# Performance work log

Hardware: AMD Instinct MI355X
Metric: run time of the kernel (lower is better)

## Reference

```python
import jax, jax.numpy as jnp
import numpy as np
from math import factorial

# ---- architecture constants (from S2ConvNet_original.__init__) ----
B_IN, B_L1, B_L2 = 30, 15, 10
F1, F2, NCLS = 20, 40, 10
BATCH = 32

# ---------- numpy precompute: Wigner small-d matrices and quadrature ----------

def wigner_d(l, beta):
    """Wigner small-d matrix d^l_{m,n}(beta) for all m,n, vectorized over beta.
    Returns [len(beta), 2l+1, 2l+1] with centered indices (row m+l, col n+l)."""
    beta = np.atleast_1d(np.asarray(beta, dtype=np.float64))
    cb, sb = np.cos(beta / 2), np.sin(beta / 2)
    d = np.zeros((beta.size, 2 * l + 1, 2 * l + 1))
    for m in range(-l, l + 1):
        for n in range(-l, l + 1):
            pref = np.sqrt(float(factorial(l + m) * factorial(l - m) * factorial(l + n) * factorial(l - n)))
            s = np.zeros_like(beta)
            for k in range(max(0, m - n), min(l + m, l - n) + 1):
                c = (-1.0) ** k / float(factorial(k) * factorial(l + m - k) * factorial(l - n - k) * factorial(n - m + k))
                s += c * cb ** (2 * l + m - n - 2 * k) * sb ** (n - m + 2 * k)
            d[:, m + l, n + l] = pref * s
    return d

def wigner_stack(nl, betas):
    """Zero-padded stack of d^l matrices: [nl, n_beta, 2nl-1, 2nl-1], centered at nl-1."""
    M, c = 2 * nl - 1, nl - 1
    D = np.zeros((nl, len(betas), M, M))
    for l in range(nl):
        D[l, :, c - l:c + l + 1, c - l:c + l + 1] = wigner_d(l, betas)
    return D

def dh_weights(b):
    """Driscoll-Healy / SOFT quadrature weights over the 2b beta samples."""
    j = np.arange(2 * b); k = np.arange(b)
    s = (np.sin(np.outer(2 * j + 1, 2 * k + 1) * np.pi / (4 * b)) / (2 * k + 1)).sum(axis=1)
    return (2.0 / b) * np.sin(np.pi * (2 * j + 1) / (4 * b)) * s

def soft_betas(b):
    return np.pi * (2 * np.arange(2 * b) + 1) / (4 * b)

def centered_freqs(nl, n):
    # map centered m in [-(nl-1), nl-1] to fft bin indices of length-n transform
    return (np.arange(2 * nl - 1) - (nl - 1)) % n

# ---- conv1 (S2 -> SO3), b_in=30, b_out=15 ----
NL1, M1 = B_L1, 2 * B_L1 - 1
_D1F = wigner_stack(NL1, soft_betas(B_IN))[:, :, :, NL1 - 1] * dh_weights(B_IN)[None, :, None]  # [15,60,29]
_D1I = wigner_stack(NL1, soft_betas(B_L1))  # [15,30,29,29]
FQI1 = centered_freqs(NL1, 2 * B_IN)
FQO1 = centered_freqs(NL1, 2 * B_L1)
# s2_near_identity_grid: max_beta=pi/8, n_alpha=8, n_beta=3 -> 24 points
_gb = np.arange(1, 4) * (np.pi / 8) / 3
_ga = np.linspace(0, 2 * np.pi, 8, endpoint=False)
GB1, GA1 = [g.ravel() for g in np.meshgrid(_gb, _ga, indexing='ij')]
_m1 = np.arange(M1) - (NL1 - 1)
_Y1 = ((2 * np.arange(NL1) + 1.0)[:, None, None]
       * wigner_stack(NL1, GB1)[:, :, :, NL1 - 1].transpose(0, 2, 1)
       * np.exp(-1j * np.outer(_m1, GA1))[None])  # [15,29,24] spherical-harmonic basis at grid

# ---- conv2 (SO3 -> SO3), b_in=15, b_out=10 ----
NL2, M2 = B_L2, 2 * B_L2 - 1
_D2F = wigner_stack(NL2, soft_betas(B_L1)) * dh_weights(B_L1)[None, :, None, None]  # [10,30,19,19]
_D2I = wigner_stack(NL2, soft_betas(B_L2))  # [10,20,19,19]
FQI2 = centered_freqs(NL2, 2 * B_L1)
FQO2 = centered_freqs(NL2, 2 * B_L2)
# so3_near_identity_grid: 3 betas x 8 alphas x 8 gammas = 192 points
_gg = np.linspace(0, 2 * np.pi, 8, endpoint=False)
GB2, GA2, GG2 = [g.ravel() for g in np.meshgrid(_gb, _ga, _gg, indexing='ij')]
_m2 = np.arange(M2) - (NL2 - 1)
_Y2 = ((2 * np.arange(NL2) + 1.0)[:, None, None, None]
       * wigner_stack(NL2, GB2).transpose(0, 2, 3, 1)
       * np.exp(-1j * (np.outer(_m2, GA2)[:, None, :] + np.outer(_m2, GG2)[None, :, :]))[None])  # [10,19,19,192]

D1F = jnp.asarray(_D1F, jnp.float32); D1I = jnp.asarray(_D1I, jnp.float32); Y1 = jnp.asarray(_Y1, jnp.complex64)
D2F = jnp.asarray(_D2F, jnp.float32); D2I = jnp.asarray(_D2I, jnp.float32); Y2 = jnp.asarray(_Y2, jnp.complex64)
W_INT = jnp.asarray(dh_weights(B_L2), jnp.float32)  # [20]


def s2_conv(x, w, bias):
    # x: [B,1,60,60] (beta, alpha) -> SO3 signal [B,F1,30,30,30]
    xf = jnp.fft.fft(x, axis=-1)[..., FQI1]                       # [B,1,60,29] alpha-FFT, centered m
    X = jnp.einsum('bfjm,ljm->bflm', xf, D1F)                      # S2 FT: [B,1,15,29]
    psi = jnp.einsum('iog,lmg->lmio', w, Y1)                       # kernel S2 FT: [15,29,1,20]
    Z = jnp.einsum('bilm,lnio->bolmn', X, jnp.conj(psi))           # outer product m x n: [B,20,15,29,29]
    Fb = jnp.einsum('bolmn,ljmn->bojmn', Z, D1I)                   # beta synthesis: [B,20,30,29,29]
    n = 2 * B_L1
    full = jnp.zeros(Fb.shape[:3] + (n, n), Fb.dtype).at[..., FQO1[:, None], FQO1[None, :]].set(Fb)
    y = jnp.fft.ifft2(full, axes=(-2, -1)).real * (n * n)          # inverse alpha/gamma FFT
    return y + bias


def so3_conv(x, w, bias):
    # x: [B,F1,30,30,30] (beta, alpha, gamma) -> [B,F2,20,20,20]
    xf = jnp.fft.fft2(x, axes=(-2, -1))[..., FQI2[:, None], FQI2[None, :]]  # [B,20,30,19,19]
    X = jnp.einsum('bfjmn,ljmn->bflmn', xf, D2F)                   # SO3 FT: [B,20,10,19,19]
    psi = jnp.einsum('iog,lmng->lmnio', w, Y2)                     # kernel SO3 FT: [10,19,19,20,40]
    Z = jnp.einsum('bilmn,lknio->bolmk', X, jnp.conj(psi))         # Z^l = X^l @ Psi^l^H: [B,40,10,19,19]
    Fb = jnp.einsum('bolmk,ljmk->bojmk', Z, D2I)                   # [B,40,20,19,19]
    n = 2 * B_L2
    full = jnp.zeros(Fb.shape[:3] + (n, n), Fb.dtype).at[..., FQO2[:, None], FQO2[None, :]].set(Fb)
    y = jnp.fft.ifft2(full, axes=(-2, -1)).real * (n * n)
    return y + bias


def setup_inputs() -> dict:
    key = jax.random.key(0)
    ks = jax.random.split(key, 6)
    x = jax.random.normal(ks[0], (BATCH, 1, 2 * B_IN, 2 * B_IN), jnp.float32)
    w1 = jax.random.normal(ks[1], (1, F1, GB1.size), jnp.float32) / np.sqrt(GB1.size)
    b1 = jax.random.normal(ks[2], (1, F1, 1, 1, 1), jnp.float32) * 0.01
    w2 = jax.random.normal(ks[3], (F1, F2, GB2.size), jnp.float32) / np.sqrt(F1 * GB2.size)
    b2 = jax.random.normal(ks[4], (1, F2, 1, 1, 1), jnp.float32) * 0.01
    w_lin = jax.random.normal(ks[5], (NCLS, F2), jnp.float32) / np.sqrt(F2)
    bl_lin = jnp.zeros((NCLS,), jnp.float32)
    return {"x": x, "w1": w1, "b1": b1, "w2": w2, "b2": b2, "w_lin": w_lin, "bl_lin": bl_lin}


def reference(x, w1, b1, w2, b2, w_lin, bl_lin):
    h = jax.nn.relu(s2_conv(x, w1, b1))                            # [B,20,30,30,30]
    h = jax.nn.relu(so3_conv(h, w2, b2))                           # [B,40,20,20,20]
    # so3_integrate: quadrature over beta, uniform sums over alpha/gamma
    g = jnp.einsum('bfjkl,j->bf', h, W_INT) * (2 * np.pi / (2 * B_L2)) ** 2
    return g @ w_lin.T + bl_lin                                    # [B,10]
```

## Files before the change

### kernel.cpp

```cpp
#include <hip/hip_runtime.h>
#include <cmath>
#include <cstdio>

#ifndef M_PI
#define M_PI 3.14159265358979323846
#endif

#define OFF_D1F 0
#define OFF_D1I 26100
#define OFF_Y1  404550
#define OFF_D2F 425430
#define OFF_D2I 533730
#define OFF_WI  605930
#define OFF_E1  605950
#define OFF_I1  609430
#define OFF_E2  611170
#define OFF_I2  612310
#define OFF_DHW30 613070
#define OFF_DHW15 613130
#define NCONST  613160

#define WOFF_CONST 0ul
#define WOFF_Y2BF  2457600ul
#define WOFF_W2BF  5406720ul
#define WOFF_AAUG  5750784ul
#define WOFF_BT    15581184ul
#define WOFF_H1    39174144ul
#define WOFF_CPSI  39174144ul
#define WOFF_Z     39174144ul
#define WOFF_H2    2457600ul
#define WOFF_XF1   76140544ul
#define WOFF_X1    (76140544ul + 445440ul)
#define WOFF_PSI1  (76140544ul + 445440ul + 111360ul)
#define WOFF_G     (76140544ul + 445440ul + 111360ul + 69600ul)
#define WS_NEED    (WOFF_G + 5120ul)

typedef __attribute__((ext_vector_type(8))) short short8v;
typedef __attribute__((ext_vector_type(4))) float f32x4;

__device__ inline unsigned short f2bf(float x){
  unsigned int u = __float_as_uint(x);
  u += 0x7FFFu + ((u >> 16) & 1u);
  return (unsigned short)(u >> 16);
}
__device__ inline float bf2f(unsigned short u){
  return __uint_as_float(((unsigned int)u) << 16);
}

__device__ inline double dfact(int n){ double r=1.0; for(int i=2;i<=n;i++) r*=(double)i; return r; }
__device__ inline double dpowi(double x,int e){ double r=1.0; for(int i=0;i<e;i++) r*=x; return r; }
__device__ double wig(int l,int m,int n,double beta){
  if(m < -l || m > l || n < -l || n > l) return 0.0;
  double cb=cos(0.5*beta), sb=sin(0.5*beta);
  double pref=sqrt(dfact(l+m)*dfact(l-m)*dfact(l+n)*dfact(l-n));
  int k0 = (m-n)>0 ? (m-n) : 0;
  int k1 = (l+m) < (l-n) ? (l+m) : (l-n);
  double c0 = ((k0&1)?-1.0:1.0)/(dfact(k0)*dfact(l+m-k0)*dfact(l-n-k0)*dfact(n-m+k0));
  double t = c0 * dpowi(cb, 2*l+m-n-2*k0) * dpowi(sb, n-m+2*k0);
  double ratio = (sb*sb)/(cb*cb);
  double s = t;
  for(int k=k0;k<k1;k++){
    t *= -((double)(l+m-k)*(double)(l-n-k)) / ((double)(k+1)*(double)(n-m+k+1)) * ratio;
    s += t;
  }
  return pref*s;
}
__device__ inline double dh_w(int b,int j){
  double s=0.0;
  for(int k=0;k<b;k++) s += sin((2.0*j+1.0)*(2.0*k+1.0)*M_PI/(4.0*b))/(2.0*k+1.0);
  return (2.0/b)*sin(M_PI*(2.0*j+1.0)/(4.0*b))*s;
}
__device__ inline double soft_beta(int b,int j){ return M_PI*(2.0*j+1.0)/(4.0*b); }
__device__ inline void octcs(int q, double* c, double* s){
  const double r = 0.70710678118654752440;
  int i = q & 7;
  const double C[8]={1.0,r,0.0,-r,-1.0,-r,0.0,r};
  const double S[8]={0.0,r,1.0,r,0.0,-r,-1.0,-r};
  *c=C[i]; *s=S[i];
}

__global__ __launch_bounds__(256) void kconst0(float* __restrict__ C){
  for(int idx = blockIdx.x*256 + threadIdx.x; idx < 3670; idx += gridDim.x*256){
    if(idx < 20){ C[OFF_WI+idx]=(float)dh_w(10,idx); }
    else if(idx < 80){ int j=idx-20; C[OFF_DHW30+j]=(float)dh_w(30,j); }
    else if(idx < 110){ int j=idx-80; C[OFF_DHW15+j]=(float)dh_w(15,j); }
    else if(idx < 1850){ int q=idx-110;
      int a=q%60; int m=q/60; double ph=-2.0*M_PI*(double)(m-14)*a/60.0;
      C[OFF_E1+2*q]=(float)cos(ph); C[OFF_E1+2*q+1]=(float)sin(ph);
    } else if(idx < 2720){ int q=idx-1850;
      int m=q%29; int p=q/29; double ph=2.0*M_PI*(double)p*(double)(m-14)/30.0;
      C[OFF_I1+2*q]=(float)cos(ph); C[OFF_I1+2*q+1]=(float)sin(ph);
    } else if(idx < 3290){ int q=idx-2720;
      int a=q%30; int m=q/30; double ph=-2.0*M_PI*(double)(m-9)*a/30.0;
      C[OFF_E2+2*q]=(float)cos(ph); C[OFF_E2+2*q+1]=(float)sin(ph);
    } else { int q=idx-3290;
      int m=q%19; int p=q/19; double ph=2.0*M_PI*(double)p*(double)(m-9)/20.0;
      C[OFF_I2+2*q]=(float)cos(ph); C[OFF_I2+2*q+1]=(float)sin(ph);
    }
  }
}

__global__ __launch_bounds__(256) void kconst(float* __restrict__ C,
                                              unsigned int* __restrict__ Y2p){
  for(long idx = (long)blockIdx.x*blockDim.x + threadIdx.x; idx < 1332770L;
      idx += (long)gridDim.x*blockDim.x){
    if(idx < 26100L){
      int m=(int)(idx%29); int j=(int)((idx/29)%60); int l=(int)(idx/(29*60));
      C[OFF_D1F+idx] = (float)( wig(l, m-14, 0, soft_beta(30,j)) * (double)C[OFF_DHW30+j] );
    } else if(idx < 404550L){ long q=idx-26100L;
      int n=(int)(q%29); int m=(int)((q/29)%29); int j=(int)((q/841)%30); int l=(int)(q/(841*30));
      C[OFF_D1I+q] = (float)wig(l, m-14, n-14, soft_beta(15,j));
    } else if(idx < 414990L){ long q=idx-404550L;
      int g=(int)(q%24); int m=(int)((q/24)%29); int l=(int)(q/(24*29));
      double gb=((g>>3)+1)*(M_PI/8.0)/3.0;
      int ka = g&7;
      double mag=(2*l+1)*wig(l, m-14, 0, gb);
      double cc,ss; octcs((m-14)*ka, &cc, &ss);
      C[OFF_Y1+2*q]  =(float)(mag*cc);
      C[OFF_Y1+2*q+1]=(float)(-mag*ss);
    } else if(idx < 523290L){ long q=idx-414990L;
      int n=(int)(q%19); int m=(int)((q/19)%19); int j=(int)((q/361)%30); int l=(int)(q/(361*30));
      C[OFF_D2F+q]=(float)( wig(l,m-9,n-9,soft_beta(15,j)) * (double)C[OFF_DHW15+j] );
    } else if(idx < 595490L){ long q=idx-523290L;
      int n=(int)(q%19); int m=(int)((q/19)%19); int j=(int)((q/361)%20); int l=(int)(q/(361*20));
      C[OFF_D2I+q]=(float)wig(l,m-9,n-9,soft_beta(10,j));
    } else { long q=idx-595490L;
      int g2=(int)(q%96); int row=(int)((q/96)%768); int l=(int)(q/(96*768));
      unsigned int outv=0u;
      if(row<722){
        int kn=row>>1, ri=row&1, kk=kn/19, n=kn%19;
        int g0=2*g2;
        double gb=((g0>>6)+1)*(M_PI/8.0)/3.0;
        double mag=(2*l+1)*wig(l,kk-9,n-9,gb);
        int ka=(g0>>3)&7;
        double c0,s0,c1,s1;
        octcs((kk-9)*ka + (n-9)*(g0&7), &c0,&s0);
        octcs((kk-9)*ka + (n-9)*((g0+1)&7), &c1,&s1);
        float v0 = ri ? (float)(-mag*s0) : (float)(mag*c0);
        float v1 = ri ? (float)(-mag*s1) : (float)(mag*c1);
        outv = (unsigned int)f2bf(v0) | (((unsigned int)f2bf(v1))<<16);
      }
      Y2p[q]=outv;
    }
  }
}

__global__ __launch_bounds__(256) void kfill(uint4* __restrict__ p, long n16){
  uint4 z; z.x=0u; z.y=0u; z.z=0u; z.w=0u;
  for(long i=(long)blockIdx.x*256+threadIdx.x; i<n16; i+=(long)gridDim.x*256) p[i]=z;
}

__global__ __launch_bounds__(256) void kw2(const float* __restrict__ w2,
                                           unsigned int* __restrict__ w2bf){
  int idx = blockIdx.x*256 + threadIdx.x;
  if(idx >= 896*96) return;
  int row=idx/96, g2=idx%96;
  float a=0.f, b=0.f;
  if(row<800){ a=w2[row*192+2*g2]; b=w2[row*192+2*g2+1]; }
  w2bf[idx] = (unsigned int)f2bf(a) | (((unsigned int)f2bf(b))<<16);
}


__global__ __launch_bounds__(256) void k1a(const float* __restrict__ x,
                                           const float2* __restrict__ E1,
                                           float2* __restrict__ xf1){
  int idx = blockIdx.x*256 + threadIdx.x;
  if(idx >= 32*60*29) return;
  int m = idx % 29; int bj = idx / 29;
  const float* row = x + bj*60;
  float sr=0.f, si=0.f;
  for(int a=0;a<60;a++){ float2 e=E1[m*60+a]; float v=row[a]; sr+=v*e.x; si+=v*e.y; }
  xf1[idx] = make_float2(sr,si);
}

__global__ __launch_bounds__(256) void k1b(const float2* __restrict__ xf1,
                                           const float* __restrict__ D1F,
                                           float2* __restrict__ X1){
  int idx = blockIdx.x*256 + threadIdx.x;
  if(idx >= 32*15*29) return;
  int m = idx % 29; int lb = idx / 29; int l = lb % 15; int b = lb / 15;
  float sr=0.f, si=0.f;
  for(int j=0;j<60;j++){
    float d = D1F[(l*60+j)*29+m]; float2 v = xf1[(b*60+j)*29+m];
    sr += d*v.x; si += d*v.y;
  }
  X1[(b*15+l)*29+m] = make_float2(sr,si);
}

__global__ __launch_bounds__(256) void kpsi1(const float* __restrict__ w1,
                                             const float2* __restrict__ Y1,
                                             float2* __restrict__ psi1cO){
  int idx = blockIdx.x*256 + threadIdx.x;
  if(idx >= 15*29*20) return;
  int o = idx % 20; int ln = idx / 20;
  float sr=0.f, si=0.f;
  for(int g=0;g<24;g++){ float w=w1[o*24+g]; float2 y=Y1[ln*24+g]; sr+=w*y.x; si+=w*y.y; }
  psi1cO[o*435 + ln] = make_float2(sr,-si);
}

__global__ __launch_bounds__(512) void k2(const float2* __restrict__ X1,
                                          const float2* __restrict__ psi1cO,
                                          const float* __restrict__ D1I,
                                          const float2* __restrict__ I1g,
                                          const float* __restrict__ b1,
                                          unsigned short* __restrict__ h1){
  int o=blockIdx.x, b=blockIdx.y;
  __shared__ float2 sX[15][29];
  __shared__ float2 sP[15][29];
  __shared__ __align__(16) unsigned short I1A[64][72];
  __shared__ __align__(16) unsigned short I1C[32][72];
  __shared__ __align__(16) unsigned short An[32][72];
  __shared__ __align__(16) unsigned short Tl[32][72];
  int t=threadIdx.x;
  for(int q=t;q<435;q+=512){ ((float2*)sX)[q]=X1[b*435+q]; ((float2*)sP)[q]=psi1cO[o*435+q]; }
  for(int q=t;q<64*72;q+=512){
    int R=q/72, k=q%72; float v=0.f;
    if(k<64){ int kk=k&31, kh=k>>5;
      if(kk<29){
        if(R<30){ float2 e=I1g[R*29+kk]; v = kh ? -e.y : e.x; }
        else if(R>=32 && R<62){ float2 e=I1g[(R-32)*29+kk]; v = kh ? e.x : e.y; }
      }
    }
    I1A[R][k]=f2bf(v);
  }
  for(int q=t;q<32*72;q+=512){
    int Qr=q/72, k=q%72; float v=0.f;
    if(Qr<30 && k<64){ int kk=k&31, kh=k>>5;
      if(kk<29){ float2 e=I1g[Qr*29+kk]; v = kh ? -e.y : e.x; }
    }
    I1C[Qr][k]=f2bf(v);
  }
  for(int q=t;q<32*72;q+=512){ An[q/72][q%72]=0; Tl[q/72][q%72]=0; }
  __syncthreads();
  float Pr[2][15], Pi[2][15];
  #pragma unroll
  for(int s=0;s<2;s++){
    int id=t+512*s;
    if(id<841){
      int m=id/29, n=id%29;
      #pragma unroll
      for(int l=0;l<15;l++){
        float2 xx=sX[l][m], pp=sP[l][n];
        Pr[s][l]=xx.x*pp.x-xx.y*pp.y;
        Pi[s][l]=xx.x*pp.y+xx.y*pp.x;
      }
    }
  }
  int wid=t>>6, lane=t&63;
  int fr=lane&15, ko=(lane>>4)*8;
  int mwB=wid>>1, nwB=wid&1;
  short8v aB0 = *(const short8v*)&I1A[16*mwB+fr][ko];
  short8v aB1 = *(const short8v*)&I1A[16*mwB+fr][32+ko];
  int mwC=(wid>>1)&1, nwC=wid&1;
  short8v bC0 = *(const short8v*)&I1C[16*nwC+fr][ko];
  short8v bC1 = *(const short8v*)&I1C[16*nwC+fr][32+ko];
  float bias=b1[o];
  for(int j=0;j<30;j++){
    #pragma unroll
    for(int s=0;s<2;s++){
      int id=t+512*s;
      if(id<841){
        const float* dp = D1I + j*841 + id;
        float ar=0.f, ai=0.f;
        #pragma unroll
        for(int l=0;l<15;l++){ float d=dp[l*25230]; ar+=Pr[s][l]*d; ai+=Pi[s][l]*d; }
        int m=id/29, n=id%29;
        An[n][m]   =f2bf(ar);
        An[n][32+m]=f2bf(ai);
      }
    }
    __syncthreads();
    f32x4 accB={0.f,0.f,0.f,0.f};
    short8v b0 = *(const short8v*)&An[16*nwB+fr][ko];
    short8v b1v= *(const short8v*)&An[16*nwB+fr][32+ko];
    accB=__builtin_amdgcn_mfma_f32_16x16x32_bf16(aB0,b0,accB,0,0,0);
    accB=__builtin_amdgcn_mfma_f32_16x16x32_bf16(aB1,b1v,accB,0,0,0);
    #pragma unroll
    for(int r=0;r<4;r++){
      int R=16*mwB+(lane>>4)*4+r;
      int cc=16*nwB+fr;
      Tl[R&31][(R>>5)*32+cc]=f2bf(accB[r]);
    }
    __syncthreads();
    if(wid<4){
      f32x4 accC={0.f,0.f,0.f,0.f};
      short8v a0 = *(const short8v*)&Tl[16*mwC+fr][ko];
      short8v a1 = *(const short8v*)&Tl[16*mwC+fr][32+ko];
      accC=__builtin_amdgcn_mfma_f32_16x16x32_bf16(a0,bC0,accC,0,0,0);
      accC=__builtin_amdgcn_mfma_f32_16x16x32_bf16(a1,bC1,accC,0,0,0);
      size_t base=((size_t)(b*20+o)*30+j)*900;
      #pragma unroll
      for(int r=0;r<4;r++){
        int p=16*mwC+(lane>>4)*4+r, qq=16*nwC+fr;
        if(p<30 && qq<30){
          float v=fmaxf(accC[r]+bias,0.f);
          h1[base+p*30+qq]=f2bf(v);
        }
      }
    }
  }
}

__global__ __launch_bounds__(256) void k3g(const unsigned short* __restrict__ A,
                                           const unsigned short* __restrict__ B,
                                           float* __restrict__ Cf){
  int l = blockIdx.z;
  int m0 = blockIdx.y*128, n0 = blockIdx.x*128;
  __shared__ unsigned short As[128][40];
  __shared__ unsigned short Bs[128][40];
  int t = threadIdx.x;
  int wid = t>>6, lane = t&63;
  int wr = wid>>1, wc = wid&1;
  f32x4 acc[4][4];
  #pragma unroll
  for(int a=0;a<4;a++)
    #pragma unroll
    for(int c=0;c<4;c++) acc[a][c]=(f32x4){0.f,0.f,0.f,0.f};
  const unsigned short* Ag = A;
  const unsigned short* Bg = B + (size_t)l*768*192;
  int row_a = wr*64 + (lane&15);
  int row_b = wc*64 + (lane&15);
  int ko = (lane>>4)*8;
  for(int kt=0; kt<192; kt+=32){
    #pragma unroll
    for(int it=0; it<2; it++){
      int q = t + 256*it;
      int r = q>>2, c8 = (q&3)*8;
      *(uint4*)&As[r][c8] = *(const uint4*)&Ag[(size_t)(m0+r)*192 + kt + c8];
      *(uint4*)&Bs[r][c8] = *(const uint4*)&Bg[(size_t)(n0+r)*192 + kt + c8];
    }
    __syncthreads();
    short8v af[4], bfv[4];
    #pragma unroll
    for(int f=0; f<4; f++){
      af[f]  = *(const short8v*)&As[row_a + f*16][ko];
      bfv[f] = *(const short8v*)&Bs[row_b + f*16][ko];
    }
    #pragma unroll
    for(int fm=0;fm<4;fm++)
      #pragma unroll
      for(int fn=0;fn<4;fn++)
        acc[fm][fn] = __builtin_amdgcn_mfma_f32_16x16x32_bf16(af[fm], bfv[fn], acc[fm][fn], 0,0,0);
    __syncthreads();
  }
  #pragma unroll
  for(int fm=0;fm<4;fm++){
    int mb = m0 + wr*64 + fm*16 + ((lane>>4)*4);
    #pragma unroll
    for(int fn=0;fn<4;fn++){
      int n = n0 + wc*64 + fn*16 + (lane&15);
      #pragma unroll
      for(int r=0;r<4;r++){
        Cf[((size_t)(l*896)+mb+r)*768 + n] = acc[fm][fn][r];
      }
    }
  }
}

__global__ __launch_bounds__(384) void kBt(const float* __restrict__ Cf,
                                           unsigned short* __restrict__ Bt){
  int c = blockIdx.x;
  int l = blockIdx.y;
  int t = threadIdx.x;
  if(t>=380) return;
  int i=t/19, n=t%19;
  int o=c/19, kk=c%19;
  float2 v = *(const float2*)&Cf[((size_t)(l*896) + i*40+o)*768 + (kk*19+n)*2];
  float zr = v.x, zi = -v.y;
  unsigned short* base = Bt + (size_t)l*1536*768;
  size_t r0=(size_t)(2*c)*768, r1=r0+768;
  int col=i*19+n;
  base[r0+col]     = f2bf(zr);
  base[r0+384+col] = f2bf(-zi);
  base[r1+col]     = f2bf(zi);
  base[r1+384+col] = f2bf(zr);
}

__global__ __launch_bounds__(512) void k4(const unsigned short* __restrict__ h1,
                                          const float* __restrict__ D2F,
                                          const float2* __restrict__ E2g,
                                          unsigned short* __restrict__ Aaug){
  int i=blockIdx.x, b=blockIdx.y;
  __shared__ __align__(16) unsigned short E2c[48][32];
  __shared__ __align__(16) unsigned short E2A[48][64];
  __shared__ __align__(16) unsigned short T1[192][72];
  __shared__ __align__(16) unsigned short U2[192][44];
  int t=threadIdx.x;
  for(int q=t;q<48*32;q+=512){
    int R=q>>5, g=q&31; float v=0.f;
    if(R<38 && g<30){ float2 e=E2g[(R%19)*30+g]; v=(R<19)? e.x : e.y; }
    E2c[R][g]=f2bf(v);
  }
  for(int q=t;q<48*64;q+=512){
    int R=q>>6, c=q&63; float v=0.f;
    if(R<38){
      int mm=R%19; int mi=(R>=19);
      if(c<30){ float2 e=E2g[mm*30+c]; v = mi ? e.y : e.x; }
      else if(c>=32 && c<62){ float2 e=E2g[mm*30+(c-32)]; v = mi ? e.x : -e.y; }
    }
    E2A[R][c]=f2bf(v);
  }
  for(int q=t;q<192*72;q+=512) T1[q/72][q%72]=0;
  for(int q=t;q<192*44;q+=512) U2[q/44][q%44]=0;
  float accr[10], acci[10];
  #pragma unroll
  for(int l=0;l<10;l++){ accr[l]=0.f; acci[l]=0.f; }
  int m3=t/19, n3=t%19;
  int wid=t>>6, lane=t&63, fr=lane&15, fc=lane&15, ko=(lane>>4)*8, rq=(lane>>4)*4;
  size_t blk=(size_t)(b*20+i)*27000;
  const unsigned int* h1u=(const unsigned int*)h1;
  __syncthreads();
  for(int p=0;p<3;p++){
    int j0=p*10;
    for(int mt=wid; mt<19; mt+=8){
      int rg=16*mt+fr;
      size_t base=blk + (size_t)j0*900 + (size_t)rg*30 + ko;
      union{ unsigned int u[4]; short8v v; } A;
      const unsigned int* pp=h1u + (base>>1);
      A.u[0]=pp[0]; A.u[1]=pp[1]; A.u[2]=pp[2]; A.u[3]=pp[3];
      #pragma unroll
      for(int nt=0;nt<3;nt++){
        short8v Bf=*(const short8v*)&E2c[16*nt+fr][ko];
        f32x4 ac={0.f,0.f,0.f,0.f};
        ac=__builtin_amdgcn_mfma_f32_16x16x32_bf16(A.v,Bf,ac,0,0,0);
        int np=16*nt+fc;
        if(np<38){
          int ri=(np>=19), nn=np-19*ri;
          #pragma unroll
          for(int r=0;r<4;r++){
            int rgw=16*mt+rq+r;
            if(rgw<300){
              int jr=rgw/30, a=rgw%30;
              T1[jr*19+nn][32*ri+a]=f2bf(ac[r]);
            }
          }
        }
      }
    }
    __syncthreads();
    for(int u=0;u<5;u++){
      int tile=wid+8*u; if(tile>=36) break;
      int mt2=tile/12, nt2=tile%12;
      short8v a0=*(const short8v*)&E2A[16*mt2+fr][ko];
      short8v a1=*(const short8v*)&E2A[16*mt2+fr][32+ko];
      short8v b0=*(const short8v*)&T1[16*nt2+fr][ko];
      short8v b1=*(const short8v*)&T1[16*nt2+fr][32+ko];
      f32x4 ac={0.f,0.f,0.f,0.f};
      ac=__builtin_amdgcn_mfma_f32_16x16x32_bf16(a0,b0,ac,0,0,0);
      ac=__builtin_amdgcn_mfma_f32_16x16x32_bf16(a1,b1,ac,0,0,0);
      int jn=16*nt2+fc;
      if(jn<190){
        #pragma unroll
        for(int r=0;r<4;r++){
          int R=16*mt2+rq+r;
          if(R<38) U2[jn][R]=f2bf(ac[r]);
        }
      }
    }
    __syncthreads();
    if(t<361){
      for(int jr=0;jr<10;jr++){
        int jg=j0+jr;
        const float* dp=D2F + (size_t)jg*361 + t;
        float xr=bf2f(U2[jr*19+n3][m3]);
        float xi=bf2f(U2[jr*19+n3][19+m3]);
        #pragma unroll
        for(int l=0;l<10;l++){ float d=dp[l*10830]; accr[l]+=d*xr; acci[l]+=d*xi; }
      }
    }
  }
  if(t<361){
    #pragma unroll
    for(int l=0;l<10;l++){
      size_t row=((size_t)(l*640) + b*19+m3)*768;
      Aaug[row + i*19+n3]       = f2bf(accr[l]);
      Aaug[row + 384 + i*19+n3] = f2bf(acci[l]);
    }
  }
}

__global__ __launch_bounds__(256) void k5(const unsigned short* __restrict__ A,
                                          const unsigned short* __restrict__ B,
                                          float* __restrict__ Cf){
  int l = blockIdx.z;
  int m0 = blockIdx.y*128, n0 = blockIdx.x*128;
  __shared__ unsigned short As[128][40];
  __shared__ unsigned short Bs[128][40];
  int t = threadIdx.x;
  int wid = t>>6, lane = t&63;
  int wr = wid>>1, wc = wid&1;
  f32x4 acc[4][4];
  #pragma unroll
  for(int a=0;a<4;a++)
    #pragma unroll
    for(int c=0;c<4;c++) acc[a][c]=(f32x4){0.f,0.f,0.f,0.f};
  const unsigned short* Ag = A + (size_t)l*640*768;
  const unsigned short* Bg = B + (size_t)l*1536*768;
  int row_a = wr*64 + (lane&15);
  int row_b = wc*64 + (lane&15);
  int ko = (lane>>4)*8;
  for(int kt=0; kt<768; kt+=32){
    #pragma unroll
    for(int it=0; it<2; it++){
      int q = t + 256*it;
      int r = q>>2, c8 = (q&3)*8;
      *(uint4*)&As[r][c8] = *(const uint4*)&Ag[(size_t)(m0+r)*768 + kt + c8];
      *(uint4*)&Bs[r][c8] = *(const uint4*)&Bg[(size_t)(n0+r)*768 + kt + c8];
    }
    __syncthreads();
    short8v af[4], bfv[4];
    #pragma unroll
    for(int f=0; f<4; f++){
      af[f]  = *(const short8v*)&As[row_a + f*16][ko];
      bfv[f] = *(const short8v*)&Bs[row_b + f*16][ko];
    }
    #pragma unroll
    for(int fm=0;fm<4;fm++)
      #pragma unroll
      for(int fn=0;fn<4;fn++)
        acc[fm][fn] = __builtin_amdgcn_mfma_f32_16x16x32_bf16(af[fm], bfv[fn], acc[fm][fn], 0,0,0);
    __syncthreads();
  }
  #pragma unroll
  for(int fm=0;fm<4;fm++){
    int mb = m0 + wr*64 + fm*16 + ((lane>>4)*4);
    #pragma unroll
    for(int fn=0;fn<4;fn++){
      int n = n0 + wc*64 + fn*16 + (lane&15);
      if(n<1520){
        #pragma unroll
        for(int r=0;r<4;r++){
          int m = mb + r;
          if(m<608) Cf[((size_t)(l*608)+m)*1520 + n] = acc[fm][fn][r];
        }
      }
    }
  }
}

__global__ __launch_bounds__(512) void k6(const float2* __restrict__ Z,
                                          const float* __restrict__ D2I,
                                          const float2* __restrict__ I2g,
                                          const float* __restrict__ b2,
                                          unsigned short* __restrict__ h2){
  int o=blockIdx.x, b=blockIdx.y;
  __shared__ __align__(16) unsigned short U[29952];
  __shared__ __align__(16) unsigned short I2A[48][72];
  __shared__ __align__(16) unsigned short I2C[32][72];
  int t=threadIdx.x;
  for(int q=t;q<14976;q+=512) ((unsigned int*)U)[q]=0u;
  for(int q=t;q<48*72;q+=512){
    int R=q/72, kd=q%72; float v=0.f;
    if(kd<38){
      int mm = (kd<19)? kd : kd-19; int hi = (kd>=19);
      if(R<20){ float2 e=I2g[R*19+mm]; v = hi ? -e.y : e.x; }
      else if(R<40){ float2 e=I2g[(R-20)*19+mm]; v = hi ? e.x : e.y; }
    }
    I2A[R][kd]=f2bf(v);
  }
  for(int q=t;q<32*72;q+=512){
    int Qr=q/72, kd=q%72; float v=0.f;
    if(Qr<20 && kd<38){
      int kk2 = (kd<19)? kd : kd-19; int hi = (kd>=19);
      float2 e=I2g[Qr*19+kk2]; v = hi ? -e.y : e.x;
    }
    I2C[Qr][kd]=f2bf(v);
  }
  float zr[10], zi[10];
  int m=t/19, kk=t%19;
  if(t<361){
    #pragma unroll
    for(int l=0;l<10;l++){
      float2 z=Z[(size_t)(l*608 + b*19+m)*760 + o*19+kk];
      zr[l]=z.x; zi[l]=z.y;
    }
  }
  __syncthreads();
  if(t<361){
    for(int j=0;j<20;j++){
      float ar=0.f, ai=0.f;
      const float* dp = D2I + j*361 + t;
      #pragma unroll
      for(int l=0;l<10;l++){ float d=dp[l*7220]; ar+=zr[l]*d; ai+=zi[l]*d; }
      U[(j*19+kk)*72 + m]      = f2bf(ar);
      U[(j*19+kk)*72 + 19 + m] = f2bf(ai);
    }
  }
  __syncthreads();
  int wid=t>>6, lane=t&63, fr=lane&15, ko=(lane>>4)*8;
  f32x4 acc1[9];
  #pragma unroll
  for(int u=0;u<9;u++){
    int tile=wid+8*u;
    int mt=tile/24, nt=tile%24;
    short8v a0=*(const short8v*)&I2A[16*mt+fr][ko];
    short8v a1=*(const short8v*)&I2A[16*mt+fr][32+ko];
    short8v bb0=*(const short8v*)&U[(16*nt+fr)*72+ko];
    short8v bb1=*(const short8v*)&U[(16*nt+fr)*72+32+ko];
    f32x4 ac={0.f,0.f,0.f,0.f};
    ac=__builtin_amdgcn_mfma_f32_16x16x32_bf16(a0,bb0,ac,0,0,0);
    ac=__builtin_amdgcn_mfma_f32_16x16x32_bf16(a1,bb1,ac,0,0,0);
    acc1[u]=ac;
  }
  __syncthreads();
  #pragma unroll
  for(int u=0;u<9;u++){
    int tile=wid+8*u; int mt=tile/24, nt=tile%24;
    #pragma unroll
    for(int r=0;r<4;r++){
      int R=16*mt+(lane>>4)*4+r;
      int n=16*nt+fr;
      if(R<40 && n<380){
        int j=n/19, kq=n%19;
        U[(j*20 + (R%20))*72 + (R/20)*19 + kq] = f2bf(acc1[u][r]);
      }
    }
  }
  __syncthreads();
  float bias=b2[o];
  size_t obase=((size_t)b*40+o)*8000;
  #pragma unroll
  for(int u=0;u<7;u++){
    int tile=wid+8*u;
    if(tile<52){
      int mt=tile>>1, nt=tile&1;
      short8v a0=*(const short8v*)&U[(16*mt+fr)*72+ko];
      short8v a1=*(const short8v*)&U[(16*mt+fr)*72+32+ko];
      short8v bb0=*(const short8v*)&I2C[16*nt+fr][ko];
      short8v bb1=*(const short8v*)&I2C[16*nt+fr][32+ko];
      f32x4 ac={0.f,0.f,0.f,0.f};
      ac=__builtin_amdgcn_mfma_f32_16x16x32_bf16(a0,bb0,ac,0,0,0);
      ac=__builtin_amdgcn_mfma_f32_16x16x32_bf16(a1,bb1,ac,0,0,0);
      #pragma unroll
      for(int r=0;r<4;r++){
        int row=16*mt+(lane>>4)*4+r;
        int q=16*nt+fr;
        if(row<400 && q<20){
          float v=fmaxf(ac[r]+bias,0.f);
          h2[obase + row*20 + q]=f2bf(v);
        }
      }
    }
  }
}

__global__ __launch_bounds__(256) void k7a(const unsigned int* __restrict__ h2p,
                                           const float* __restrict__ WI,
                                           float* __restrict__ g){
  int bf=blockIdx.x;
  const unsigned int* base=h2p + (size_t)bf*4000;
  int t=threadIdx.x; float s=0.f;
  for(int q=t;q<4000;q+=256){
    unsigned int v=base[q];
    float w=WI[q/200];
    s += (bf2f((unsigned short)(v&0xFFFF))+bf2f((unsigned short)(v>>16)))*w;
  }
  __shared__ float red[256];
  red[t]=s; __syncthreads();
  for(int off=128;off>0;off>>=1){ if(t<off) red[t]+=red[t+off]; __syncthreads(); }
  if(t==0){
    const float c=(float)((2.0*M_PI/20.0)*(2.0*M_PI/20.0));
    g[bf]=red[0]*c;
  }
}

__global__ __launch_bounds__(64) void k7b(const float* __restrict__ g,
                                          const float* __restrict__ wlin,
                                          const float* __restrict__ bl,
                                          float* __restrict__ out){
  int idx=blockIdx.x*64+threadIdx.x;
  if(idx>=320) return;
  int b=idx/10, c=idx%10;
  float s=bl[c];
  for(int f=0;f<40;f++) s += g[b*40+f]*wlin[c*40+f];
  out[b*10+c]=s;
}

extern "C" void kernel_launch(void* const* d_in, const int* in_sizes, int n_in,
                              void* d_out, int out_size, void* d_ws, size_t ws_size,
                              hipStream_t stream){
  (void)in_sizes; (void)n_in; (void)out_size;
  const float* x    = (const float*)d_in[0];
  const float* w1   = (const float*)d_in[1];
  const float* b1   = (const float*)d_in[2];
  const float* w2   = (const float*)d_in[3];
  const float* b2   = (const float*)d_in[4];
  const float* wlin = (const float*)d_in[5];
  const float* bl   = (const float*)d_in[6];
  float* out = (float*)d_out;
  char*  ws  = (char*)d_ws;

  if(ws_size < WS_NEED){
    fprintf(stderr, "kernel_launch: ws too small: have %zu need %lu\n", ws_size, WS_NEED);
  }

  float* C = (float*)(ws + WOFF_CONST);
  const float*  D1F = C + OFF_D1F;
  const float*  D1I = C + OFF_D1I;
  const float2* Y1  = (const float2*)(C + OFF_Y1);
  const float*  D2F = C + OFF_D2F;
  const float*  D2I = C + OFF_D2I;
  const float*  WI  = C + OFF_WI;
  const float2* E1  = (const float2*)(C + OFF_E1);
  const float2* I1  = (const float2*)(C + OFF_I1);
  const float2* E2  = (const float2*)(C + OFF_E2);
  const float2* I2  = (const float2*)(C + OFF_I2);

  float2* xf1   = (float2*)(ws + WOFF_XF1);
  float2* X1    = (float2*)(ws + WOFF_X1);
  float2* psi1c = (float2*)(ws + WOFF_PSI1);
  unsigned short* h1   = (unsigned short*)(ws + WOFF_H1);
  unsigned short* Y2bf = (unsigned short*)(ws + WOFF_Y2BF);
  unsigned short* w2bf = (unsigned short*)(ws + WOFF_W2BF);
  float*  Cpsi  = (float*)(ws + WOFF_CPSI);
  unsigned short* Aaug = (unsigned short*)(ws + WOFF_AAUG);
  unsigned short* Bt   = (unsigned short*)(ws + WOFF_BT);
  float*  Zf    = (float*)(ws + WOFF_Z);
  unsigned short* h2 = (unsigned short*)(ws + WOFF_H2);
  float*  g     = (float*)(ws + WOFF_G);

  hipLaunchKernelGGL(kconst0, dim3(16), dim3(256), 0, stream, C);
  hipLaunchKernelGGL(kconst, dim3(2048), dim3(256), 0, stream, C, (unsigned int*)Y2bf);
  hipLaunchKernelGGL(kfill, dim3(2048), dim3(256), 0, stream,
                     (uint4*)(ws + WOFF_AAUG), (long)(33423360ul/16ul));
  hipLaunchKernelGGL(kfill, dim3(1), dim3(256), 0, stream,
                     (uint4*)(ws + WOFF_H1 + 34560000ul), 32L);
  hipLaunchKernelGGL(kw2, dim3((896*96+255)/256), dim3(256), 0, stream, w2, (unsigned int*)w2bf);

  hipLaunchKernelGGL(k1a, dim3((32*60*29+255)/256), dim3(256), 0, stream, x, E1, xf1);
  hipLaunchKernelGGL(k1b, dim3((32*15*29+255)/256), dim3(256), 0, stream, xf1, D1F, X1);
  hipLaunchKernelGGL(kpsi1, dim3((15*29*20+255)/256), dim3(256), 0, stream, w1, Y1, psi1c);
  hipLaunchKernelGGL(k2, dim3(20,32), dim3(512), 0, stream, X1, psi1c, D1I, I1, b1, h1);
  hipLaunchKernelGGL(k4, dim3(20,32), dim3(512), 0, stream, h1, D2F, E2, Aaug);
  hipLaunchKernelGGL(k3g, dim3(6,7,10), dim3(256), 0, stream, w2bf, Y2bf, Cpsi);
  hipLaunchKernelGGL(kBt, dim3(760,10), dim3(384), 0, stream, Cpsi, Bt);
  hipLaunchKernelGGL(k5, dim3(12,5,10), dim3(256), 0, stream, Aaug, Bt, Zf);
  hipLaunchKernelGGL(k6, dim3(40,32), dim3(512), 0, stream, (const float2*)Zf, D2I, I2, b2, h2);
  hipLaunchKernelGGL(k7a, dim3(1280), dim3(256), 0, stream, (const unsigned int*)h2, WI, g);
  hipLaunchKernelGGL(k7b, dim3(5), dim3(64), 0, stream, g, wlin, bl, out);
}
```

Baseline: 435.4 us.

## Split k2 beta loop across grid z and batch six betas per block

The k2 kernel previously looped over all 30 output beta samples in each block, with two barriers per beta. It now launches 5 blocks along z, each handling 6 betas. Each block computes all 6 Wigner-combined slices into a shared buffer, then runs the two MFMA stages across all betas, with only three barriers total. This raises grid parallelism (640 to 3200 blocks) and cuts synchronisation. The cost is redundant setup per block (loading the I1 tables and computing the P products) and more shared memory and registers.

```diff
diff --git a/kernel.cpp b/kernel.cpp
--- a/kernel.cpp
+++ b/kernel.cpp
@@ -198,19 +198,19 @@
   psi1cO[o*435 + ln] = make_float2(sr,-si);
 }
 
+#define JC 6
 __global__ __launch_bounds__(512) void k2(const float2* __restrict__ X1,
                                           const float2* __restrict__ psi1cO,
                                           const float* __restrict__ D1I,
                                           const float2* __restrict__ I1g,
                                           const float* __restrict__ b1,
                                           unsigned short* __restrict__ h1){
-  int o=blockIdx.x, b=blockIdx.y;
+  int o=blockIdx.x, b=blockIdx.y, j0=blockIdx.z*JC;
   __shared__ float2 sX[15][29];
   __shared__ float2 sP[15][29];
   __shared__ __align__(16) unsigned short I1A[64][72];
   __shared__ __align__(16) unsigned short I1C[32][72];
-  __shared__ __align__(16) unsigned short An[32][72];
-  __shared__ __align__(16) unsigned short Tl[32][72];
+  __shared__ __align__(16) unsigned short U[JC*32*72];
   int t=threadIdx.x;
   for(int q=t;q<435;q+=512){ ((float2*)sX)[q]=X1[b*435+q]; ((float2*)sP)[q]=psi1cO[o*435+q]; }
   for(int q=t;q<64*72;q+=512){
@@ -230,7 +230,7 @@
     }
     I1C[Qr][k]=f2bf(v);
   }
-  for(int q=t;q<32*72;q+=512){ An[q/72][q%72]=0; Tl[q/72][q%72]=0; }
+  for(int q=t;q<JC*32*36;q+=512) ((unsigned int*)U)[q]=0u;
   __syncthreads();
   float Pr[2][15], Pi[2][15];
   #pragma unroll
@@ -247,53 +247,70 @@
     }
   }
   int wid=t>>6, lane=t&63;
-  int fr=lane&15, ko=(lane>>4)*8;
-  int mwB=wid>>1, nwB=wid&1;
-  short8v aB0 = *(const short8v*)&I1A[16*mwB+fr][ko];
-  short8v aB1 = *(const short8v*)&I1A[16*mwB+fr][32+ko];
-  int mwC=(wid>>1)&1, nwC=wid&1;
-  short8v bC0 = *(const short8v*)&I1C[16*nwC+fr][ko];
-  short8v bC1 = *(const short8v*)&I1C[16*nwC+fr][32+ko];
+  int fr=lane&15, fc=lane&15, rq=(lane>>4)*4, ko=(lane>>4)*8;
   float bias=b1[o];
-  for(int j=0;j<30;j++){
-    #pragma unroll
-    for(int s=0;s<2;s++){
-      int id=t+512*s;
-      if(id<841){
-        const float* dp = D1I + j*841 + id;
+  #pragma unroll
+  for(int s=0;s<2;s++){
+    int id=t+512*s;
+    if(id<841){
+      int m=id/29, n=id%29;
+      for(int jr=0;jr<JC;jr++){
+        const float* dp = D1I + (j0+jr)*841 + id;
         float ar=0.f, ai=0.f;
         #pragma unroll
         for(int l=0;l<15;l++){ float d=dp[l*25230]; ar+=Pr[s][l]*d; ai+=Pi[s][l]*d; }
-        int m=id/29, n=id%29;
-        An[n][m]   =f2bf(ar);
-        An[n][32+m]=f2bf(ai);
-      }
-    }
-    __syncthreads();
-    f32x4 accB={0.f,0.f,0.f,0.f};
-    short8v b0 = *(const short8v*)&An[16*nwB+fr][ko];
-    short8v b1v= *(const short8v*)&An[16*nwB+fr][32+ko];
-    accB=__builtin_amdgcn_mfma_f32_16x16x32_bf16(aB0,b0,accB,0,0,0);
-    accB=__builtin_amdgcn_mfma_f32_16x16x32_bf16(aB1,b1v,accB,0,0,0);
+        U[(jr*32+n)*72 + m]    = f2bf(ar);
+        U[(jr*32+n)*72 + 32+m] = f2bf(ai);
+      }
+    }
+  }
+  __syncthreads();
+  f32x4 accB[JC];
+  #pragma unroll
+  for(int u=0;u<JC;u++){
+    int tile = wid + 8*u;
+    int mt = tile/(2*JC), nt = tile%(2*JC);
+    short8v a0=*(const short8v*)&I1A[16*mt+fr][ko];
+    short8v a1=*(const short8v*)&I1A[16*mt+fr][32+ko];
+    short8v b0=*(const short8v*)&U[(16*nt+fr)*72+ko];
+    short8v b1=*(const short8v*)&U[(16*nt+fr)*72+32+ko];
+    f32x4 ac={0.f,0.f,0.f,0.f};
+    ac=__builtin_amdgcn_mfma_f32_16x16x32_bf16(a0,b0,ac,0,0,0);
+    ac=__builtin_amdgcn_mfma_f32_16x16x32_bf16(a1,b1,ac,0,0,0);
+    accB[u]=ac;
+  }
+  __syncthreads();
+  #pragma unroll
+  for(int u=0;u<JC;u++){
+    int tile = wid + 8*u;
+    int mt = tile/(2*JC), nt = tile%(2*JC);
     #pragma unroll
     for(int r=0;r<4;r++){
-      int R=16*mwB+(lane>>4)*4+r;
-      int cc=16*nwB+fr;
-      Tl[R&31][(R>>5)*32+cc]=f2bf(accB[r]);
-    }
-    __syncthreads();
-    if(wid<4){
-      f32x4 accC={0.f,0.f,0.f,0.f};
-      short8v a0 = *(const short8v*)&Tl[16*mwC+fr][ko];
-      short8v a1 = *(const short8v*)&Tl[16*mwC+fr][32+ko];
-      accC=__builtin_amdgcn_mfma_f32_16x16x32_bf16(a0,bC0,accC,0,0,0);
-      accC=__builtin_amdgcn_mfma_f32_16x16x32_bf16(a1,bC1,accC,0,0,0);
-      size_t base=((size_t)(b*20+o)*30+j)*900;
+      int R=16*mt+rq+r;
+      int jn=16*nt+fc;
+      int p=R&31, hi=R>>5, jj=jn>>5, n=jn&31;
+      U[p*(JC*64) + jj*64 + hi*32 + n] = f2bf(accB[u][r]);
+    }
+  }
+  __syncthreads();
+  #pragma unroll
+  for(int u=0;u<(4*JC+7)/8;u++){
+    int tile = wid + 8*u;
+    if(tile < 4*JC){
+      int jj=tile>>2, sub=tile&3, mtC=sub>>1, ntC=sub&1;
+      short8v a0=*(const short8v*)&U[(16*mtC+fr)*(JC*64) + jj*64 + ko];
+      short8v a1=*(const short8v*)&U[(16*mtC+fr)*(JC*64) + jj*64 + 32 + ko];
+      short8v b0=*(const short8v*)&I1C[16*ntC+fr][ko];
+      short8v b1=*(const short8v*)&I1C[16*ntC+fr][32+ko];
+      f32x4 ac={0.f,0.f,0.f,0.f};
+      ac=__builtin_amdgcn_mfma_f32_16x16x32_bf16(a0,b0,ac,0,0,0);
+      ac=__builtin_amdgcn_mfma_f32_16x16x32_bf16(a1,b1,ac,0,0,0);
+      size_t base=((size_t)(b*20+o)*30+(j0+jj))*900;
       #pragma unroll
       for(int r=0;r<4;r++){
-        int p=16*mwC+(lane>>4)*4+r, qq=16*nwC+fr;
+        int p=16*mtC+rq+r, qq=16*ntC+fc;
         if(p<30 && qq<30){
-          float v=fmaxf(accC[r]+bias,0.f);
+          float v=fmaxf(ac[r]+bias,0.f);
           h1[base+p*30+qq]=f2bf(v);
         }
       }
@@ -730,7 +747,7 @@
   hipLaunchKernelGGL(k1a, dim3((32*60*29+255)/256), dim3(256), 0, stream, x, E1, xf1);
   hipLaunchKernelGGL(k1b, dim3((32*15*29+255)/256), dim3(256), 0, stream, xf1, D1F, X1);
   hipLaunchKernelGGL(kpsi1, dim3((15*29*20+255)/256), dim3(256), 0, stream, w1, Y1, psi1c);
-  hipLaunchKernelGGL(k2, dim3(20,32), dim3(512), 0, stream, X1, psi1c, D1I, I1, b1, h1);
+  hipLaunchKernelGGL(k2, dim3(20,32,5), dim3(512), 0, stream, X1, psi1c, D1I, I1, b1, h1);
   hipLaunchKernelGGL(k4, dim3(20,32), dim3(512), 0, stream, h1, D2F, E2, Aaug);
   hipLaunchKernelGGL(k3g, dim3(6,7,10), dim3(256), 0, stream, w2bf, Y2bf, Cpsi);
   hipLaunchKernelGGL(kBt, dim3(760,10), dim3(384), 0, stream, Cpsi, Bt);
```

Result: no change. 433.9 us (-0.3%).
